# Kernel tuning notes

Hardware: AMD Instinct MI355X
Metric: run time of the kernel (lower is better)

Reference implementation:

```python
import jax, jax.numpy as jnp
import numpy as np

B, S, IN_DIM, HID, H, CS = 4, 4096, 1024, 1024, 16, 16
HD = HID // H
LN_EPS = 1e-5


def setup_inputs() -> dict:
    key = jax.random.key(0)
    ks = jax.random.split(key, 6)
    x = jax.random.normal(ks[0], (B, S, IN_DIM), jnp.float32)
    W_in = jax.random.normal(ks[1], (HID, IN_DIM), jnp.float32) * (IN_DIM ** -0.5)
    ln_g = jnp.ones((HID,), jnp.float32)
    ln_b = jnp.zeros((HID,), jnp.float32)
    W_gate = jax.random.normal(ks[2], (2 * H, HID), jnp.float32) * (HID ** -0.5)
    b_gate = jnp.zeros((2 * H,), jnp.float32)
    raw = 0.5 * float(np.log(1.9 / 0.1))  # atanh(0.9), as in _init_eigenvalues
    eig_raw = jnp.full((H,), raw, jnp.float32) + 0.01 * jax.random.normal(ks[3], (H,), jnp.float32)
    W_out = jax.random.normal(ks[4], (HID, HID), jnp.float32) * (HID ** -0.5)
    return {"x": x, "W_in": W_in, "ln_g": ln_g, "ln_b": ln_b,
            "W_gate": W_gate, "b_gate": b_gate, "eig_raw": eig_raw, "W_out": W_out}


def _chunk_scan(a, b):
    # a: (B,S,H) decay, b: (B,S,H,HD) input; h_t = a_t*h_{t-1} + b_t, h0 = 0
    Bsz, Sl = a.shape[0], a.shape[1]
    N = Sl // CS  # seq_len chosen divisible by chunk_size (pad_len == 0)
    ac = a.reshape(Bsz, N, CS, H)
    bc = b.reshape(Bsz, N, CS, H, HD)
    cum = jnp.cumprod(ac, axis=2)  # (B,N,C,H)
    ones = jnp.ones((Bsz, N, 1, H), a.dtype)
    cum_pad = jnp.concatenate([ones, cum[:, :, :-1]], axis=2)  # shifted cumprod
    # M[i,j] = cum_i / cum_pad_j for i>j, 1 on diag, 0 above
    Mi = cum[:, :, :, None, :]        # (B,N,C,1,H)
    Mj = cum_pad[:, :, None, :, :]    # (B,N,1,C,H)
    M = jnp.where(jnp.abs(Mj) > 1e-8, Mi / Mj, jnp.zeros_like(Mi))
    tril = jnp.tril(jnp.ones((CS, CS), a.dtype))[None, None, :, :, None]
    eye = jnp.eye(CS, dtype=a.dtype)[None, None, :, :, None]
    M = M * tril
    M = M * (1 - eye) + eye  # force exact 1 on diagonal
    # within-chunk contribution: (B,N,C,H,HD)
    h_contrib = jnp.einsum('bnijh,bnjhd->bnihd', M, bc)
    # inter-chunk sequential carry
    cum_T = jnp.moveaxis(cum, 1, 0)            # (N,B,C,H)
    hc_T = jnp.moveaxis(h_contrib, 1, 0)       # (N,B,C,H,HD)

    def step(h, inp):
        cum_n, hc_n = inp
        h_chunk = cum_n[..., None] * h[:, None] + hc_n  # (B,C,H,HD)
        return h_chunk[:, -1], h_chunk

    h0 = jnp.zeros((Bsz, H, HD), a.dtype)
    _, h_all = jax.lax.scan(step, h0, (cum_T, hc_T))   # (N,B,C,H,HD)
    h_all = jnp.moveaxis(h_all, 0, 1).reshape(Bsz, Sl, HID)
    return h_all


def reference(x, W_in, ln_g, ln_b, W_gate, b_gate, eig_raw, W_out):
    Bsz, Sl, _ = x.shape
    xp = x @ W_in.T                               # (B,S,HID)
    mu = jnp.mean(xp, axis=-1, keepdims=True)
    var = jnp.mean((xp - mu) ** 2, axis=-1, keepdims=True)
    xp = (xp - mu) * jax.lax.rsqrt(var + LN_EPS) * ln_g + ln_b
    gates = xp @ W_gate.T + b_gate                # (B,S,2H)
    alpha = jax.nn.sigmoid(gates[..., :H])
    beta = jax.nn.sigmoid(gates[..., H:])
    eig = jnp.tanh(eig_raw)                       # (H,)
    a = eig[None, None, :] * alpha                # (B,S,H)
    x_heads = xp.reshape(Bsz, Sl, H, HD)
    b = beta[..., None] * x_heads                 # (B,S,H,HD)
    h_all = _chunk_scan(a, b)                     # (B,S,HID)
    output = h_all @ W_out.T                      # dropout is identity in eval
    h_final = h_all[:, -1, :]
    return output, h_final
```

## Files before the change

### kernel.cpp

```cpp
#include <hip/hip_runtime.h>
#include <hip/hip_bf16.h>
#include <stdint.h>

#define BATCH 4
#define SEQ   4096
#define HID   1024
#define NH    16
#define HD    64
#define CS    16
#define NCH   256
#define MROWS 16384

typedef __attribute__((ext_vector_type(8))) __bf16 bf16x8;
typedef __attribute__((ext_vector_type(4))) float  f32x4;

__device__ __forceinline__ unsigned short f2bf(float f) {
    union { float f; unsigned u; } x; x.f = f;
    unsigned r = x.u + 0x7FFFu + ((x.u >> 16) & 1u);
    return (unsigned short)(r >> 16);
}
__device__ __forceinline__ float bf2f(unsigned short v) {
    union { unsigned u; float f; } x; x.u = ((unsigned)v) << 16;
    return x.f;
}

__device__ __forceinline__ void async_copy16(void* lds, const void* g) {
    __builtin_amdgcn_global_load_lds(
        (const __attribute__((address_space(1))) unsigned int*)g,
        (__attribute__((address_space(3))) unsigned int*)lds,
        16, 0, 0);
}

__global__ __launch_bounds__(256) void convert_all_kernel(
    const float* __restrict__ x, const float* __restrict__ W_in,
    const float* __restrict__ W_out, const float* __restrict__ W_gate,
    unsigned short* __restrict__ xb, unsigned short* __restrict__ Wib,
    unsigned short* __restrict__ Wob, unsigned short* __restrict__ WgT)
{
    int i = blockIdx.x * 256 + threadIdx.x;
    if (i < 4194304) {
        float4 v = ((const float4*)x)[i];
        ushort4 o;
        o.x = f2bf(v.x); o.y = f2bf(v.y); o.z = f2bf(v.z); o.w = f2bf(v.w);
        ((ushort4*)xb)[i] = o;
    } else if (i < 4456448) {
        int j = i - 4194304;
        float4 v = ((const float4*)W_in)[j];
        ushort4 o;
        o.x = f2bf(v.x); o.y = f2bf(v.y); o.z = f2bf(v.z); o.w = f2bf(v.w);
        ((ushort4*)Wib)[j] = o;
    } else if (i < 4718592) {
        int j = i - 4456448;
        float4 v = ((const float4*)W_out)[j];
        ushort4 o;
        o.x = f2bf(v.x); o.y = f2bf(v.y); o.z = f2bf(v.z); o.w = f2bf(v.w);
        ((ushort4*)Wob)[j] = o;
    } else if (i < 4726784) {
        int j = i - 4718592;
        int g  = j >> 8;
        int kq = j & 255;
        float4 v = ((const float4*)W_gate)[g * 256 + kq];
        int k0 = kq * 4;
        WgT[(k0 + 0) * 32 + g] = f2bf(v.x);
        WgT[(k0 + 1) * 32 + g] = f2bf(v.y);
        WgT[(k0 + 2) * 32 + g] = f2bf(v.z);
        WgT[(k0 + 3) * 32 + g] = f2bf(v.w);
    }
}

__global__ __launch_bounds__(256, 2) void gemm_bt_kernel(
    const unsigned short* __restrict__ A,
    const unsigned short* __restrict__ Bm,
    float* __restrict__ C, int M, int N, int K)
{
    __shared__ unsigned short As[128 * 64];
    __shared__ unsigned short Bs[128 * 64];
    const int t = threadIdx.x;
    const int lane = t & 63, w = t >> 6;
    const int wm = w >> 1, wn = w & 1;
    const size_t bm = (size_t)blockIdx.x * 128;
    const size_t bn = (size_t)blockIdx.y * 128;

    f32x4 acc[4][4];
#pragma unroll
    for (int x = 0; x < 4; x++)
#pragma unroll
        for (int y = 0; y < 4; y++)
            acc[x][y] = (f32x4){0.f, 0.f, 0.f, 0.f};

    const int srow = lane >> 3;
    const int gc   = (lane & 7) ^ (srow & 7);
    const int scol = gc * 8;
    const unsigned short* Ag = A + (bm + w * 32 + srow) * (size_t)K + scol;
    const unsigned short* Bg = Bm + (bn + w * 32 + srow) * (size_t)K + scol;
    unsigned short* Al = As + (w * 32 + srow) * 64 + (lane & 7) * 8;
    unsigned short* Bl = Bs + (w * 32 + srow) * 64 + (lane & 7) * 8;

    const int fr = lane & 15, fq = lane >> 4;
    const int rl = fr & 7;

    for (int k0 = 0; k0 < K; k0 += 64) {
#pragma unroll
        for (int r = 0; r < 4; r++) {
            async_copy16(Al + r * 8 * 64, Ag + (size_t)r * 8 * K + k0);
            async_copy16(Bl + r * 8 * 64, Bg + (size_t)r * 8 * K + k0);
        }
        __syncthreads();
#pragma unroll
        for (int kk = 0; kk < 64; kk += 32) {
            const int c = (kk >> 3) + fq;
            const int pc = c ^ rl;
            bf16x8 af[4], bfv[4];
#pragma unroll
            for (int x = 0; x < 4; x++) {
                af[x]  = *(const bf16x8*)(As + (wm * 64 + x * 16 + fr) * 64 + pc * 8);
                bfv[x] = *(const bf16x8*)(Bs + (wn * 64 + x * 16 + fr) * 64 + pc * 8);
            }
#pragma unroll
            for (int x = 0; x < 4; x++)
#pragma unroll
                for (int y = 0; y < 4; y++)
                    acc[x][y] = __builtin_amdgcn_mfma_f32_16x16x32_bf16(af[x], bfv[y], acc[x][y], 0, 0, 0);
        }
        __syncthreads();
    }

#pragma unroll
    for (int x = 0; x < 4; x++) {
#pragma unroll
        for (int y = 0; y < 4; y++) {
            size_t r0 = bm + wm * 64 + x * 16 + fq * 4;
            size_t c  = bn + wn * 64 + y * 16 + fr;
#pragma unroll
            for (int rg = 0; rg < 4; rg++)
                C[(r0 + rg) * (size_t)N + c] = acc[x][y][rg];
        }
    }
}

__global__ __launch_bounds__(256) void mid_kernel(
    const float* __restrict__ xp,
    const float* __restrict__ ln_g, const float* __restrict__ ln_b,
    const unsigned short* __restrict__ WgT,
    const float* __restrict__ bg, const float* __restrict__ eig_raw,
    unsigned short* __restrict__ xln,
    float* __restrict__ beta_buf,
    float* __restrict__ cum_out,
    float* __restrict__ c15c,
    float* __restrict__ hc15)
{
    __shared__ unsigned short sx[16][1032];
    __shared__ unsigned short swg[1024 * 32];
    __shared__ float sg[16][32];
    __shared__ float scum[16][16];
    __shared__ float sm15[16][16];
    const int t = threadIdx.x;
    const int bn = blockIdx.x;
    const size_t m0 = (size_t)(bn >> 8) * SEQ + (size_t)(bn & 255) * 16;

#pragma unroll
    for (int i = 0; i < 16; i++)
        async_copy16((char*)swg + (i * 256 + t) * 16, (const char*)WgT + (i * 256 + t) * 16);

    const int r = t >> 4, u = t & 15;
    const float* row = xp + (m0 + r) * 1024;
    float4 v[16];
    float s = 0.f, s2 = 0.f;
#pragma unroll
    for (int i = 0; i < 16; i++) {
        v[i] = *(const float4*)(row + u * 4 + i * 64);
        s  += v[i].x + v[i].y + v[i].z + v[i].w;
        s2 += v[i].x * v[i].x + v[i].y * v[i].y + v[i].z * v[i].z + v[i].w * v[i].w;
    }
#pragma unroll
    for (int off = 1; off < 16; off <<= 1) {
        s  += __shfl_xor(s, off, 64);
        s2 += __shfl_xor(s2, off, 64);
    }
    const float mu = s * (1.f / 1024.f);
    const float var = s2 * (1.f / 1024.f) - mu * mu;
    const float sc = rsqrtf(var + 1e-5f);
    unsigned short* orow = xln + (m0 + r) * 1024;
#pragma unroll
    for (int i = 0; i < 16; i++) {
        const int k = u * 4 + i * 64;
        float4 g4 = *(const float4*)(ln_g + k);
        float4 b4 = *(const float4*)(ln_b + k);
        ushort4 o;
        o.x = f2bf((v[i].x - mu) * sc * g4.x + b4.x);
        o.y = f2bf((v[i].y - mu) * sc * g4.y + b4.y);
        o.z = f2bf((v[i].z - mu) * sc * g4.z + b4.z);
        o.w = f2bf((v[i].w - mu) * sc * g4.w + b4.w);
        *(ushort4*)&sx[r][k] = o;
        *(ushort4*)(orow + k) = o;
    }
    __syncthreads();

    {
        const int r2 = t >> 4, jg = t & 15;
        float a0 = 0.f, a1 = 0.f;
        for (int k8 = 0; k8 < 1024; k8 += 8) {
            ushort4 xa = *(const ushort4*)&sx[r2][k8];
            ushort4 xb2 = *(const ushort4*)&sx[r2][k8 + 4];
            float xf[8] = { bf2f(xa.x), bf2f(xa.y), bf2f(xa.z), bf2f(xa.w),
                            bf2f(xb2.x), bf2f(xb2.y), bf2f(xb2.z), bf2f(xb2.w) };
#pragma unroll
            for (int kk = 0; kk < 8; kk++) {
                unsigned wpair = *(const unsigned*)&swg[(k8 + kk) * 32 + 2 * jg];
                a0 += xf[kk] * bf2f((unsigned short)(wpair & 0xffff));
                a1 += xf[kk] * bf2f((unsigned short)(wpair >> 16));
            }
        }
        const float g0 = a0 + bg[2 * jg];
        const float g1 = a1 + bg[2 * jg + 1];
        sg[r2][2 * jg]     = 1.f / (1.f + expf(-g0));
        sg[r2][2 * jg + 1] = 1.f / (1.f + expf(-g1));
    }
    __syncthreads();

    if (t < 16) {
        const float ev = tanhf(eig_raw[t]);
        float c = 1.f;
#pragma unroll
        for (int i = 0; i < 16; i++) { c *= ev * sg[i][t]; scum[i][t] = c; }
    }
    {
        const int rr = t >> 4, h = t & 15;
        beta_buf[(m0 + rr) * 16 + h] = sg[rr][16 + h];
    }
    __syncthreads();

    {
        const int j = t >> 4, h = t & 15;
        const float cum15 = scum[15][h];
        const float cpad = (j == 0) ? 1.f : scum[j - 1][h];
        float mv;
        if (j == 15) mv = 1.f;
        else mv = (fabsf(cpad) > 1e-8f) ? (cum15 / cpad) : 0.f;
        sm15[j][h] = mv * sg[j][16 + h];
        cum_out[(size_t)bn * 256 + t] = scum[j][h];
        if (t < 16) c15c[bn * 16 + t] = scum[15][t];
    }
    __syncthreads();

    {
        const int h = t >> 4, d0 = (t & 15) * 4;
        float a0 = 0.f, a1 = 0.f, a2 = 0.f, a3 = 0.f;
#pragma unroll
        for (int j = 0; j < 16; j++) {
            const float m = sm15[j][h];
            ushort4 bv = *(const ushort4*)&sx[j][h * 64 + d0];
            a0 += m * bf2f(bv.x); a1 += m * bf2f(bv.y);
            a2 += m * bf2f(bv.z); a3 += m * bf2f(bv.w);
        }
        float4 o = { a0, a1, a2, a3 };
        *(float4*)(hc15 + (size_t)bn * 1024 + h * 64 + d0) = o;
    }
}

__global__ __launch_bounds__(256) void scan2_kernel(
    const float* __restrict__ c15c,
    const float* __restrict__ hc15,
    float* __restrict__ carry_in,
    float* __restrict__ h_final)
{
    const int p = blockIdx.x * 256 + threadIdx.x;
    const int b = p >> 10, hd = p & 1023, h = hd >> 6;
    float carry = 0.f;
#pragma unroll 8
    for (int n = 0; n < NCH; n++) {
        const size_t bn = (size_t)b * NCH + n;
        const float c15 = c15c[bn * 16 + h];
        carry_in[bn * 1024 + hd] = carry;
        carry = c15 * carry + hc15[bn * 1024 + hd];
    }
    h_final[(size_t)b * 1024 + hd] = carry;
}

__global__ __launch_bounds__(256) void scan3_kernel(
    const float* __restrict__ cum_buf,
    const float* __restrict__ beta_buf,
    const unsigned short* __restrict__ xln,
    const float* __restrict__ carry_in,
    unsigned short* __restrict__ hall)
{
    __shared__ float scum[16][16];
    __shared__ float sbeta[16][16];
    __shared__ float sm[16][16][16];
    __shared__ unsigned short sx[16][1024];
    const int t = threadIdx.x;
    const int bn = blockIdx.x;
    const size_t m0 = (size_t)(bn >> 8) * SEQ + (size_t)(bn & 255) * 16;

    scum[t >> 4][t & 15]  = cum_buf[(size_t)bn * 256 + t];
    sbeta[t >> 4][t & 15] = beta_buf[(m0 + (t >> 4)) * 16 + (t & 15)];
#pragma unroll
    for (int i = 0; i < 16; i++)
        *(ushort4*)&sx[i][t * 4] = *(const ushort4*)(xln + (m0 + i) * 1024 + t * 4);
    __syncthreads();

    {
        const int i = t >> 4, h = t & 15;
        const float ci = scum[i][h];
#pragma unroll
        for (int j = 0; j < 16; j++) {
            float mv;
            if (j > i) mv = 0.f;
            else if (j == i) mv = 1.f;
            else {
                const float cpad = (j == 0) ? 1.f : scum[j - 1][h];
                mv = (fabsf(cpad) > 1e-8f) ? (ci / cpad) : 0.f;
            }
            sm[i][j][h] = mv * sbeta[j][h];
        }
    }
    __syncthreads();

    {
        const int h = t >> 4, d0 = (t & 15) * 4;
        float4 car = *(const float4*)(carry_in + (size_t)bn * 1024 + h * 64 + d0);
#pragma unroll
        for (int i = 0; i < 16; i++) {
            float a0 = 0.f, a1 = 0.f, a2 = 0.f, a3 = 0.f;
            for (int j = 0; j <= i; j++) {
                const float m = sm[i][j][h];
                ushort4 bv = *(const ushort4*)&sx[j][h * 64 + d0];
                a0 += m * bf2f(bv.x); a1 += m * bf2f(bv.y);
                a2 += m * bf2f(bv.z); a3 += m * bf2f(bv.w);
            }
            const float ci = scum[i][h];
            ushort4 o;
            o.x = f2bf(ci * car.x + a0);
            o.y = f2bf(ci * car.y + a1);
            o.z = f2bf(ci * car.z + a2);
            o.w = f2bf(ci * car.w + a3);
            *(ushort4*)(hall + (m0 + i) * 1024 + h * 64 + d0) = o;
        }
    }
}

extern "C" void kernel_launch(void* const* d_in, const int* in_sizes, int n_in,
                              void* d_out, int out_size, void* d_ws, size_t ws_size,
                              hipStream_t stream)
{
    const float* x       = (const float*)d_in[0];
    const float* W_in    = (const float*)d_in[1];
    const float* ln_g    = (const float*)d_in[2];
    const float* ln_b    = (const float*)d_in[3];
    const float* W_gate  = (const float*)d_in[4];
    const float* b_gate  = (const float*)d_in[5];
    const float* eig_raw = (const float*)d_in[6];
    const float* W_out   = (const float*)d_in[7];
    float* out = (float*)d_out;

    char* ws = (char*)d_ws;
    unsigned short* xb   = (unsigned short*)(ws);
    unsigned short* xln  = (unsigned short*)(ws);
    unsigned short* hall = (unsigned short*)(ws + 33554432);
    unsigned short* Wib  = (unsigned short*)(ws + 67108864);
    unsigned short* Wob  = (unsigned short*)(ws + 69206016);
    unsigned short* WgT  = (unsigned short*)(ws + 71303168);
    float* beta_buf = (float*)(ws + 71368704);
    float* cum_buf  = (float*)(ws + 72417280);
    float* c15c     = (float*)(ws + 73465856);
    float* hc15     = (float*)(ws + 73531392);
    float* carry_in = (float*)(ws + 77725696);

    float* xp = out;
    float* h_final = out + 16777216;

    convert_all_kernel<<<18464, 256, 0, stream>>>(x, W_in, W_out, W_gate, xb, Wib, Wob, WgT);

    dim3 gg(128, 8);
    gemm_bt_kernel<<<gg, 256, 0, stream>>>(xb, Wib, xp, MROWS, HID, HID);

    mid_kernel<<<1024, 256, 0, stream>>>(xp, ln_g, ln_b, WgT, b_gate, eig_raw,
                                         xln, beta_buf, cum_buf, c15c, hc15);

    scan2_kernel<<<16, 256, 0, stream>>>(c15c, hc15, carry_in, h_final);
    scan3_kernel<<<1024, 256, 0, stream>>>(cum_buf, beta_buf, xln, carry_in, hall);

    gemm_bt_kernel<<<gg, 256, 0, stream>>>(hall, Wob, out, MROWS, HID, HID);
}
```

Measured before the change: 314.7 us.

## Compute gate projection with MFMA and drop the LDS-staged transposed gate weights

The gate GEMV in mid_kernel, previously done with scalar FMAs over a 64 KB LDS copy of the transposed gate weights, now runs on bf16 16x16x32 MFMA instructions. Each of the four waves handles a quarter of K, reading weights directly from global memory, and the partial sums are reduced through a small LDS buffer. This cuts LDS usage a lot, which should raise occupancy, and makes the weight conversion a plain cast. Separately, scan2 is relaunched as 64 blocks of 64 threads to spread the serial carry scan over more CUs.

```diff
diff --git a/kernel.cpp b/kernel.cpp
--- a/kernel.cpp
+++ b/kernel.cpp
@@ -35,37 +35,19 @@
     const float* __restrict__ x, const float* __restrict__ W_in,
     const float* __restrict__ W_out, const float* __restrict__ W_gate,
     unsigned short* __restrict__ xb, unsigned short* __restrict__ Wib,
-    unsigned short* __restrict__ Wob, unsigned short* __restrict__ WgT)
+    unsigned short* __restrict__ Wob, unsigned short* __restrict__ Wgb)
 {
     int i = blockIdx.x * 256 + threadIdx.x;
-    if (i < 4194304) {
-        float4 v = ((const float4*)x)[i];
-        ushort4 o;
-        o.x = f2bf(v.x); o.y = f2bf(v.y); o.z = f2bf(v.z); o.w = f2bf(v.w);
-        ((ushort4*)xb)[i] = o;
-    } else if (i < 4456448) {
-        int j = i - 4194304;
-        float4 v = ((const float4*)W_in)[j];
-        ushort4 o;
-        o.x = f2bf(v.x); o.y = f2bf(v.y); o.z = f2bf(v.z); o.w = f2bf(v.w);
-        ((ushort4*)Wib)[j] = o;
-    } else if (i < 4718592) {
-        int j = i - 4456448;
-        float4 v = ((const float4*)W_out)[j];
-        ushort4 o;
-        o.x = f2bf(v.x); o.y = f2bf(v.y); o.z = f2bf(v.z); o.w = f2bf(v.w);
-        ((ushort4*)Wob)[j] = o;
-    } else if (i < 4726784) {
-        int j = i - 4718592;
-        int g  = j >> 8;
-        int kq = j & 255;
-        float4 v = ((const float4*)W_gate)[g * 256 + kq];
-        int k0 = kq * 4;
-        WgT[(k0 + 0) * 32 + g] = f2bf(v.x);
-        WgT[(k0 + 1) * 32 + g] = f2bf(v.y);
-        WgT[(k0 + 2) * 32 + g] = f2bf(v.z);
-        WgT[(k0 + 3) * 32 + g] = f2bf(v.w);
-    }
+    const float4* src; ushort4* dst; int j;
+    if (i < 4194304)      { src = (const float4*)x;      dst = (ushort4*)xb;  j = i; }
+    else if (i < 4456448) { src = (const float4*)W_in;   dst = (ushort4*)Wib; j = i - 4194304; }
+    else if (i < 4718592) { src = (const float4*)W_out;  dst = (ushort4*)Wob; j = i - 4456448; }
+    else if (i < 4726784) { src = (const float4*)W_gate; dst = (ushort4*)Wgb; j = i - 4718592; }
+    else return;
+    float4 v = src[j];
+    ushort4 o;
+    o.x = f2bf(v.x); o.y = f2bf(v.y); o.z = f2bf(v.z); o.w = f2bf(v.w);
+    dst[j] = o;
 }
 
 __global__ __launch_bounds__(256, 2) void gemm_bt_kernel(
@@ -141,7 +123,7 @@
 __global__ __launch_bounds__(256) void mid_kernel(
     const float* __restrict__ xp,
     const float* __restrict__ ln_g, const float* __restrict__ ln_b,
-    const unsigned short* __restrict__ WgT,
+    const unsigned short* __restrict__ Wgb,
     const float* __restrict__ bg, const float* __restrict__ eig_raw,
     unsigned short* __restrict__ xln,
     float* __restrict__ beta_buf,
@@ -150,71 +132,82 @@
     float* __restrict__ hc15)
 {
     __shared__ unsigned short sx[16][1032];
-    __shared__ unsigned short swg[1024 * 32];
+    __shared__ float red[4][2][64][4];
     __shared__ float sg[16][32];
     __shared__ float scum[16][16];
     __shared__ float sm15[16][16];
-    const int t = threadIdx.x;
+    const int t = threadIdx.x, lane = t & 63, w = t >> 6;
     const int bn = blockIdx.x;
     const size_t m0 = (size_t)(bn >> 8) * SEQ + (size_t)(bn & 255) * 16;
 
-#pragma unroll
-    for (int i = 0; i < 16; i++)
-        async_copy16((char*)swg + (i * 256 + t) * 16, (const char*)WgT + (i * 256 + t) * 16);
-
     const int r = t >> 4, u = t & 15;
-    const float* row = xp + (m0 + r) * 1024;
-    float4 v[16];
-    float s = 0.f, s2 = 0.f;
-#pragma unroll
-    for (int i = 0; i < 16; i++) {
-        v[i] = *(const float4*)(row + u * 4 + i * 64);
-        s  += v[i].x + v[i].y + v[i].z + v[i].w;
-        s2 += v[i].x * v[i].x + v[i].y * v[i].y + v[i].z * v[i].z + v[i].w * v[i].w;
-    }
-#pragma unroll
-    for (int off = 1; off < 16; off <<= 1) {
-        s  += __shfl_xor(s, off, 64);
-        s2 += __shfl_xor(s2, off, 64);
-    }
-    const float mu = s * (1.f / 1024.f);
-    const float var = s2 * (1.f / 1024.f) - mu * mu;
-    const float sc = rsqrtf(var + 1e-5f);
-    unsigned short* orow = xln + (m0 + r) * 1024;
-#pragma unroll
-    for (int i = 0; i < 16; i++) {
-        const int k = u * 4 + i * 64;
-        float4 g4 = *(const float4*)(ln_g + k);
-        float4 b4 = *(const float4*)(ln_b + k);
-        ushort4 o;
-        o.x = f2bf((v[i].x - mu) * sc * g4.x + b4.x);
-        o.y = f2bf((v[i].y - mu) * sc * g4.y + b4.y);
-        o.z = f2bf((v[i].z - mu) * sc * g4.z + b4.z);
-        o.w = f2bf((v[i].w - mu) * sc * g4.w + b4.w);
-        *(ushort4*)&sx[r][k] = o;
-        *(ushort4*)(orow + k) = o;
-    }
-    __syncthreads();
-
-    {
-        const int r2 = t >> 4, jg = t & 15;
-        float a0 = 0.f, a1 = 0.f;
-        for (int k8 = 0; k8 < 1024; k8 += 8) {
-            ushort4 xa = *(const ushort4*)&sx[r2][k8];
-            ushort4 xb2 = *(const ushort4*)&sx[r2][k8 + 4];
-            float xf[8] = { bf2f(xa.x), bf2f(xa.y), bf2f(xa.z), bf2f(xa.w),
-                            bf2f(xb2.x), bf2f(xb2.y), bf2f(xb2.z), bf2f(xb2.w) };
-#pragma unroll
-            for (int kk = 0; kk < 8; kk++) {
-                unsigned wpair = *(const unsigned*)&swg[(k8 + kk) * 32 + 2 * jg];
-                a0 += xf[kk] * bf2f((unsigned short)(wpair & 0xffff));
-                a1 += xf[kk] * bf2f((unsigned short)(wpair >> 16));
-            }
-        }
-        const float g0 = a0 + bg[2 * jg];
-        const float g1 = a1 + bg[2 * jg + 1];
-        sg[r2][2 * jg]     = 1.f / (1.f + expf(-g0));
-        sg[r2][2 * jg + 1] = 1.f / (1.f + expf(-g1));
+    {
+        const float* row = xp + (m0 + r) * 1024;
+        float4 v[16];
+        float s = 0.f, s2 = 0.f;
+#pragma unroll
+        for (int i = 0; i < 16; i++) {
+            v[i] = *(const float4*)(row + u * 4 + i * 64);
+            s  += v[i].x + v[i].y + v[i].z + v[i].w;
+            s2 += v[i].x * v[i].x + v[i].y * v[i].y + v[i].z * v[i].z + v[i].w * v[i].w;
+        }
+#pragma unroll
+        for (int off = 1; off < 16; off <<= 1) {
+            s  += __shfl_xor(s, off, 64);
+            s2 += __shfl_xor(s2, off, 64);
+        }
+        const float mu = s * (1.f / 1024.f);
+        const float var = s2 * (1.f / 1024.f) - mu * mu;
+        const float sc = rsqrtf(var + 1e-5f);
+        unsigned short* orow = xln + (m0 + r) * 1024;
+#pragma unroll
+        for (int i = 0; i < 16; i++) {
+            const int k = u * 4 + i * 64;
+            float4 g4 = *(const float4*)(ln_g + k);
+            float4 b4 = *(const float4*)(ln_b + k);
+            ushort4 o;
+            o.x = f2bf((v[i].x - mu) * sc * g4.x + b4.x);
+            o.y = f2bf((v[i].y - mu) * sc * g4.y + b4.y);
+            o.z = f2bf((v[i].z - mu) * sc * g4.z + b4.z);
+            o.w = f2bf((v[i].w - mu) * sc * g4.w + b4.w);
+            *(ushort4*)&sx[r][k] = o;
+            *(ushort4*)(orow + k) = o;
+        }
+    }
+    __syncthreads();
+
+    const int fr = lane & 15, fq = lane >> 4;
+    {
+        f32x4 acc0 = (f32x4){0.f,0.f,0.f,0.f}, acc1 = (f32x4){0.f,0.f,0.f,0.f};
+        const unsigned short* Wr0 = Wgb + (size_t)fr * 1024;
+        const unsigned short* Wr1 = Wgb + (size_t)(16 + fr) * 1024;
+#pragma unroll
+        for (int ks = 0; ks < 8; ks++) {
+            const int k0 = w * 256 + ks * 32 + fq * 8;
+            bf16x8 af = *(const bf16x8*)&sx[fr][k0];
+            bf16x8 b0 = *(const bf16x8*)(Wr0 + k0);
+            bf16x8 b1 = *(const bf16x8*)(Wr1 + k0);
+            acc0 = __builtin_amdgcn_mfma_f32_16x16x32_bf16(af, b0, acc0, 0, 0, 0);
+            acc1 = __builtin_amdgcn_mfma_f32_16x16x32_bf16(af, b1, acc1, 0, 0, 0);
+        }
+        *(f32x4*)&red[w][0][lane][0] = acc0;
+        *(f32x4*)&red[w][1][lane][0] = acc1;
+    }
+    __syncthreads();
+    if (t < 128) {
+        const int y = t >> 6, l = t & 63;
+        f32x4 s = *(const f32x4*)&red[0][y][l][0];
+#pragma unroll
+        for (int ww = 1; ww < 4; ww++) {
+            f32x4 p = *(const f32x4*)&red[ww][y][l][0];
+            s[0] += p[0]; s[1] += p[1]; s[2] += p[2]; s[3] += p[3];
+        }
+        const int col = y * 16 + (l & 15);
+        const int row0 = (l >> 4) * 4;
+        const float bias = bg[col];
+#pragma unroll
+        for (int rg = 0; rg < 4; rg++)
+            sg[row0 + rg][col] = 1.f / (1.f + expf(-(s[rg] + bias)));
     }
     __syncthreads();
 
@@ -224,10 +217,7 @@
 #pragma unroll
         for (int i = 0; i < 16; i++) { c *= ev * sg[i][t]; scum[i][t] = c; }
     }
-    {
-        const int rr = t >> 4, h = t & 15;
-        beta_buf[(m0 + rr) * 16 + h] = sg[rr][16 + h];
-    }
+    beta_buf[(m0 + r) * 16 + u] = sg[r][16 + u];
     __syncthreads();
 
     {
@@ -258,13 +248,13 @@
     }
 }
 
-__global__ __launch_bounds__(256) void scan2_kernel(
+__global__ __launch_bounds__(64) void scan2_kernel(
     const float* __restrict__ c15c,
     const float* __restrict__ hc15,
     float* __restrict__ carry_in,
     float* __restrict__ h_final)
 {
-    const int p = blockIdx.x * 256 + threadIdx.x;
+    const int p = blockIdx.x * 64 + threadIdx.x;
     const int b = p >> 10, hd = p & 1023, h = hd >> 6;
     float carry = 0.f;
 #pragma unroll 8
@@ -359,7 +349,7 @@
     unsigned short* hall = (unsigned short*)(ws + 33554432);
     unsigned short* Wib  = (unsigned short*)(ws + 67108864);
     unsigned short* Wob  = (unsigned short*)(ws + 69206016);
-    unsigned short* WgT  = (unsigned short*)(ws + 71303168);
+    unsigned short* Wgb  = (unsigned short*)(ws + 71303168);
     float* beta_buf = (float*)(ws + 71368704);
     float* cum_buf  = (float*)(ws + 72417280);
     float* c15c     = (float*)(ws + 73465856);
@@ -369,15 +359,15 @@
     float* xp = out;
     float* h_final = out + 16777216;
 
-    convert_all_kernel<<<18464, 256, 0, stream>>>(x, W_in, W_out, W_gate, xb, Wib, Wob, WgT);
+    convert_all_kernel<<<18464, 256, 0, stream>>>(x, W_in, W_out, W_gate, xb, Wib, Wob, Wgb);
 
     dim3 gg(128, 8);
     gemm_bt_kernel<<<gg, 256, 0, stream>>>(xb, Wib, xp, MROWS, HID, HID);
 
-    mid_kernel<<<1024, 256, 0, stream>>>(xp, ln_g, ln_b, WgT, b_gate, eig_raw,
+    mid_kernel<<<1024, 256, 0, stream>>>(xp, ln_g, ln_b, Wgb, b_gate, eig_raw,
                                          xln, beta_buf, cum_buf, c15c, hc15);
 
-    scan2_kernel<<<16, 256, 0, stream>>>(c15c, hc15, carry_in, h_final);
+    scan2_kernel<<<64, 64, 0, stream>>>(c15c, hc15, carry_in, h_final);
     scan3_kernel<<<1024, 256, 0, stream>>>(cum_buf, beta_buf, xln, carry_in, hall);
 
     gemm_bt_kernel<<<gg, 256, 0, stream>>>(hall, Wob, out, MROWS, HID, HID);
```

Result: faster. 272.8 us (-13.3%).
